# Optimization experiments

Hardware: AMD Instinct MI355X
Metric: run time of the kernel (lower is better)

Reference implementation:

```python
import jax, jax.numpy as jnp
import numpy as np
from jax import lax

B, N, F_IN, T = 4, 30000, 2, 12
HID, HORIZON, E = 32, 12, 240000


def setup_inputs() -> dict:
    key = jax.random.key(0)
    ks = jax.random.split(key, 20)

    def lin_init(k, fan_in, shape):
        b = 1.0 / np.sqrt(fan_in)
        return jax.random.uniform(k, shape, jnp.float32, -b, b)

    def glorot(k, shape):
        b = np.sqrt(6.0 / (shape[0] + shape[1]))
        return jax.random.uniform(k, shape, jnp.float32, -b, b)

    return {
        "x": jax.random.normal(ks[0], (B, N, F_IN, T), jnp.float32),
        "edge_index": jax.random.randint(ks[1], (2, E), 0, N, jnp.int32),
        # A3TGCN2 attention over periods (init: uniform[0,1))
        "attention": jax.random.uniform(ks[2], (T,), jnp.float32),
        # TGCN2 gates: GCNConv weight (F_IN,HID) + bias, Linear (2*HID,HID) + bias
        "conv_z_w": glorot(ks[3], (F_IN, HID)), "conv_z_b": jnp.zeros((HID,), jnp.float32),
        "lin_z_w": lin_init(ks[4], 2 * HID, (2 * HID, HID)), "lin_z_b": lin_init(ks[5], 2 * HID, (HID,)),
        "conv_r_w": glorot(ks[6], (F_IN, HID)), "conv_r_b": jnp.zeros((HID,), jnp.float32),
        "lin_r_w": lin_init(ks[7], 2 * HID, (2 * HID, HID)), "lin_r_b": lin_init(ks[8], 2 * HID, (HID,)),
        "conv_h_w": glorot(ks[9], (F_IN, HID)), "conv_h_b": jnp.zeros((HID,), jnp.float32),
        "lin_h_w": lin_init(ks[10], 2 * HID, (2 * HID, HID)), "lin_h_b": lin_init(ks[11], 2 * HID, (HID,)),
        # trailing head Linear(HID, HORIZON)
        "head_w": lin_init(ks[12], HID, (HID, HORIZON)), "head_b": lin_init(ks[13], HID, (HORIZON,)),
    }


def _forward(x, attention, conv_z_w, conv_z_b, lin_z_w, lin_z_b,
             conv_r_w, conv_r_b, lin_r_w, lin_r_b,
             conv_h_w, conv_h_b, lin_h_w, lin_h_b,
             head_w, head_b, edge_index):
    b, n = x.shape[0], x.shape[1]
    # GCN normalization with added self loops: D^-1/2 (A+I) D^-1/2
    loop = jnp.arange(n, dtype=edge_index.dtype)
    src = jnp.concatenate([edge_index[0], loop])  # (E+N,) message sources
    dst = jnp.concatenate([edge_index[1], loop])  # (E+N,) message targets
    deg = jnp.zeros((n,), x.dtype).at[dst].add(1.0)  # deg >= 1 due to self loops
    dinv = lax.rsqrt(deg)
    norm = dinv[src] * dinv[dst]  # (E+N,)

    def gcn(xt, W, bias):
        # xt: (B,N,F) -> (B,N,HID); gather from src, scatter-add to dst
        xw = jnp.einsum('bnf,fh->bnh', xt, W)
        msg = xw[:, src, :] * norm[None, :, None]  # (B,E+N,HID)
        agg = jnp.zeros((b, n, W.shape[1]), xt.dtype).at[:, dst, :].add(msg)
        return agg + bias

    probs = jax.nn.softmax(attention)  # (T,)
    H0 = jnp.zeros((b, n, HID), x.dtype)  # A3TGCN2 passes H=None every period

    def step(acc, inps):
        xt, p = inps  # xt: (B,N,F)
        Z = jax.nn.sigmoid(jnp.concatenate([gcn(xt, conv_z_w, conv_z_b), H0], -1) @ lin_z_w + lin_z_b)
        R = jax.nn.sigmoid(jnp.concatenate([gcn(xt, conv_r_w, conv_r_b), H0], -1) @ lin_r_w + lin_r_b)
        Ht = jnp.tanh(jnp.concatenate([gcn(xt, conv_h_w, conv_h_b), H0 * R], -1) @ lin_h_w + lin_h_b)
        Hn = Z * H0 + (1.0 - Z) * Ht
        return acc + p * Hn, None

    acc, _ = lax.scan(step, H0, (jnp.moveaxis(x, 3, 0), probs))
    return jax.nn.relu(acc) @ head_w + head_b  # (B,N,HORIZON)


def reference(x, edge_index, attention, conv_z_w, conv_z_b, lin_z_w, lin_z_b,
              conv_r_w, conv_r_b, lin_r_w, lin_r_b,
              conv_h_w, conv_h_b, lin_h_w, lin_h_b, head_w, head_b):
    return _forward(x, attention, conv_z_w, conv_z_b, lin_z_w, lin_z_b,
                    conv_r_w, conv_r_b, lin_r_w, lin_r_b,
                    conv_h_w, conv_h_b, lin_h_w, lin_h_b,
                    head_w, head_b, edge_index)
```

## Files before the change

kernel.cpp:

```cpp
#include <hip/hip_runtime.h>

#define BB   4
#define NN   30000
#define TT   12
#define EE   240000
#define FT   24
#define NM   96
#define CAP  32
#define OVCAP 2048
#define FB   ((EE + 255) / 256)
#define LOG2E 1.44269504088896340736f

#define WS_CNT 0
#define WS_OVC 30000
#define WS_EFF 30016
#define WS_OVF 30272
#define WS_BKT 34368

__device__ __forceinline__ float readlane_f(float v, int l) {
    return __int_as_float(__builtin_amdgcn_readlane(__float_as_int(v), l));
}

__global__ void __launch_bounds__(256)
k_pre(const int* __restrict__ src, const int* __restrict__ dst,
      const float* __restrict__ czw, const float* __restrict__ czb,
      const float* __restrict__ lzw, const float* __restrict__ lzb,
      const float* __restrict__ chw, const float* __restrict__ chb,
      const float* __restrict__ lhw, const float* __restrict__ lhb,
      const float* __restrict__ att,
      int* __restrict__ cnt, int* __restrict__ ovc,
      int* __restrict__ ovf, int* __restrict__ bucket, float* __restrict__ eff) {
    int bid = blockIdx.x, lt = threadIdx.x;
    if (bid < FB) {
        int e = bid * 256 + lt;
        if (e < EE) {
            int d = dst[e], s = src[e];
            int slot = atomicAdd(&cnt[d], 1);
            if (slot < CAP) {
                bucket[d * CAP + slot] = s;
            } else {
                int o = atomicAdd(ovc, 1);
                if (o < OVCAP) { ovf[2 * o] = d; ovf[2 * o + 1] = s; }
            }
        }
        return;
    }
    int j = lt;
    if (j < 32) {
        float wz0 = 0.f, wz1 = 0.f, bz = 0.f, wh0 = 0.f, wh1 = 0.f, bh = 0.f;
        for (int k = 0; k < 32; ++k) {
            float lz = lzw[k * 32 + j], lh = lhw[k * 32 + j];
            wz0 = fmaf(czw[k],      lz, wz0);
            wz1 = fmaf(czw[32 + k], lz, wz1);
            bz  = fmaf(czb[k],      lz, bz);
            wh0 = fmaf(chw[k],      lh, wh0);
            wh1 = fmaf(chw[32 + k], lh, wh1);
            bh  = fmaf(chb[k],      lh, bh);
        }
        eff[j]        = -LOG2E * wz0;
        eff[32 + j]   = -LOG2E * wz1;
        eff[64 + j]   = -LOG2E * (bz + lzb[j]);
        eff[96 + j]   = 2.0f * LOG2E * wh0;
        eff[128 + j]  = 2.0f * LOG2E * wh1;
        eff[160 + j]  = 2.0f * LOG2E * (bh + lhb[j]);
    } else if (j == 32) {
        float m = -1e30f;
        for (int t = 0; t < TT; ++t) m = fmaxf(m, att[t]);
        float p[TT], s = 0.f;
        for (int t = 0; t < TT; ++t) { p[t] = __expf(att[t] - m); s += p[t]; }
        float inv = 1.0f / s;
        for (int t = 0; t < TT; ++t) eff[192 + t] = p[t] * inv;
    }
}

__global__ void __launch_bounds__(128)
k_fused(const float* __restrict__ x, const int* __restrict__ cnt,
        const int* __restrict__ ovc, const int* __restrict__ ovf,
        const int* __restrict__ bucket, const float* __restrict__ eff,
        const float* __restrict__ hw, const float* __restrict__ hb,
        float* __restrict__ out) {
    __shared__ float se[204];
    __shared__ float shwT[432];
    __shared__ float shb[12];
    __shared__ float sx[2 * NM];
    __shared__ float lacc[2 * 4 * 36];
    const int lt = threadIdx.x, lane = lt & 63, w = lt >> 6;
    const int n = blockIdx.x * 2 + w;

    for (int i = lt; i < 204; i += 128) se[i] = eff[i];
    if (lt < 12) shb[lt] = hb[lt];
    for (int i = lt; i < 384; i += 128) {
        int jj = i / 12, kk = i - 12 * jj;
        shwT[kk * 36 + jj] = hw[i];
    }
    __syncthreads();

    const bool act = (lane < 48);
    const int b = lane / 12, f2 = lane - 12 * b;
    const float2* xb = (const float2*)x;
    const int lane_off = b * (NN * 12) + f2;

    const int deg = __builtin_amdgcn_readfirstlane(cnt[n]);
    const int m = (deg < CAP) ? deg : CAP;
    int sv = (lane < m) ? bucket[n * CAP + lane] : n;
    float wv = (lane <= m) ? rsqrtf((float)(cnt[sv] + 1)) : 0.f;

    float2 acc = {0.f, 0.f};
    const int total = m + 1;
    int k = 0;
    for (; k + 8 <= total; k += 8) {
        int s0 = __builtin_amdgcn_readlane(sv, k);
        int s1 = __builtin_amdgcn_readlane(sv, k + 1);
        int s2 = __builtin_amdgcn_readlane(sv, k + 2);
        int s3 = __builtin_amdgcn_readlane(sv, k + 3);
        int s4 = __builtin_amdgcn_readlane(sv, k + 4);
        int s5 = __builtin_amdgcn_readlane(sv, k + 5);
        int s6 = __builtin_amdgcn_readlane(sv, k + 6);
        int s7 = __builtin_amdgcn_readlane(sv, k + 7);
        if (act) {
            float2 v0 = xb[lane_off + s0 * 12];
            float2 v1 = xb[lane_off + s1 * 12];
            float2 v2 = xb[lane_off + s2 * 12];
            float2 v3 = xb[lane_off + s3 * 12];
            float2 v4 = xb[lane_off + s4 * 12];
            float2 v5 = xb[lane_off + s5 * 12];
            float2 v6 = xb[lane_off + s6 * 12];
            float2 v7 = xb[lane_off + s7 * 12];
            float w0 = readlane_f(wv, k),     w1 = readlane_f(wv, k + 1);
            float w2 = readlane_f(wv, k + 2), w3 = readlane_f(wv, k + 3);
            float w4 = readlane_f(wv, k + 4), w5 = readlane_f(wv, k + 5);
            float w6 = readlane_f(wv, k + 6), w7 = readlane_f(wv, k + 7);
            acc.x = fmaf(w0, v0.x, acc.x); acc.y = fmaf(w0, v0.y, acc.y);
            acc.x = fmaf(w1, v1.x, acc.x); acc.y = fmaf(w1, v1.y, acc.y);
            acc.x = fmaf(w2, v2.x, acc.x); acc.y = fmaf(w2, v2.y, acc.y);
            acc.x = fmaf(w3, v3.x, acc.x); acc.y = fmaf(w3, v3.y, acc.y);
            acc.x = fmaf(w4, v4.x, acc.x); acc.y = fmaf(w4, v4.y, acc.y);
            acc.x = fmaf(w5, v5.x, acc.x); acc.y = fmaf(w5, v5.y, acc.y);
            acc.x = fmaf(w6, v6.x, acc.x); acc.y = fmaf(w6, v6.y, acc.y);
            acc.x = fmaf(w7, v7.x, acc.x); acc.y = fmaf(w7, v7.y, acc.y);
        }
    }
    for (; k < total; k += 4) {
        int s0 = __builtin_amdgcn_readlane(sv, k);
        int s1 = __builtin_amdgcn_readlane(sv, k + 1);
        int s2 = __builtin_amdgcn_readlane(sv, k + 2);
        int s3 = __builtin_amdgcn_readlane(sv, k + 3);
        if (act) {
            float2 v0 = xb[lane_off + s0 * 12];
            float2 v1 = xb[lane_off + s1 * 12];
            float2 v2 = xb[lane_off + s2 * 12];
            float2 v3 = xb[lane_off + s3 * 12];
            float w0 = readlane_f(wv, k),     w1 = readlane_f(wv, k + 1);
            float w2 = readlane_f(wv, k + 2), w3 = readlane_f(wv, k + 3);
            acc.x = fmaf(w0, v0.x, acc.x); acc.y = fmaf(w0, v0.y, acc.y);
            acc.x = fmaf(w1, v1.x, acc.x); acc.y = fmaf(w1, v1.y, acc.y);
            acc.x = fmaf(w2, v2.x, acc.x); acc.y = fmaf(w2, v2.y, acc.y);
            acc.x = fmaf(w3, v3.x, acc.x); acc.y = fmaf(w3, v3.y, acc.y);
        }
    }

    int nov = __builtin_amdgcn_readfirstlane(*ovc);
    if (nov > 0) {
        if (nov > OVCAP) nov = OVCAP;
        for (int i = 0; i < nov; ++i) {
            int d = ovf[2 * i];
            if (d == n) {
                int s = ovf[2 * i + 1];
                float ws_ = rsqrtf((float)(cnt[s] + 1));
                if (act) {
                    float2 v = xb[lane_off + s * 12];
                    acc.x = fmaf(ws_, v.x, acc.x);
                    acc.y = fmaf(ws_, v.y, acc.y);
                }
            }
        }
    }

    const float dn = readlane_f(wv, m);
    if (act) {
        float2* sx2 = (float2*)(sx + w * NM + b * FT);
        sx2[f2] = make_float2(dn * acc.x, dn * acc.y);
    }
    __builtin_amdgcn_wave_barrier();

    const int j = lane & 31, b0_ = lane >> 5;
    const float az0 = se[j],      az1 = se[32 + j],  ab = se[64 + j];
    const float ch0 = se[96 + j], ch1 = se[128 + j], cb = se[160 + j];
#pragma unroll
    for (int bi = 0; bi < 2; ++bi) {
        const int bb = b0_ + 2 * bi;
        const float4* s4 = (const float4*)(sx + w * NM + bb * FT);
        float4 q[6];
#pragma unroll
        for (int i = 0; i < 6; ++i) q[i] = s4[i];
        const float* av = (const float*)q;
        float a = 0.f;
#pragma unroll
        for (int t = 0; t < TT; ++t) {
            float v0 = av[t], v1 = av[12 + t], pp = se[192 + t];
            float ae = fmaf(v1, az1, fmaf(v0, az0, ab));
            float ce = fmaf(v1, ch1, fmaf(v0, ch0, cb));
            ae = __builtin_amdgcn_fmed3f(ae, -126.f, 126.f);
            ce = __builtin_amdgcn_fmed3f(ce, -126.f, 126.f);
            float u  = __builtin_amdgcn_exp2f(ae);
            float e2 = __builtin_amdgcn_exp2f(ce);
            float t1_ = 1.0f + u;
            float den = fmaf(e2, t1_, t1_);
            float num = fmaf(u, e2, -u);
            float r   = __builtin_amdgcn_rcpf(den);
            a = fmaf(pp * num, r, a);
        }
        lacc[(w * 4 + bb) * 36 + j] = fmaxf(a, 0.f);
    }
    __builtin_amdgcn_wave_barrier();

    if (lane < 48) {
        int bb = lane / 12, kk = lane - 12 * bb;
        float r = shb[kk];
        const float4* la4 = (const float4*)(lacc + (w * 4 + bb) * 36);
        const float4* wt4 = (const float4*)(shwT + kk * 36);
#pragma unroll
        for (int i = 0; i < 8; ++i) {
            float4 a4 = la4[i], w4 = wt4[i];
            r = fmaf(a4.x, w4.x, r); r = fmaf(a4.y, w4.y, r);
            r = fmaf(a4.z, w4.z, r); r = fmaf(a4.w, w4.w, r);
        }
        out[((long long)bb * NN + n) * 12 + kk] = r;
    }
}

extern "C" void kernel_launch(void* const* d_in, const int* in_sizes, int n_in,
                              void* d_out, int out_size, void* d_ws, size_t ws_size,
                              hipStream_t stream) {
    const float* x   = (const float*)d_in[0];
    const int*   ei  = (const int*)d_in[1];
    const float* att = (const float*)d_in[2];
    const float* czw = (const float*)d_in[3];
    const float* czb = (const float*)d_in[4];
    const float* lzw = (const float*)d_in[5];
    const float* lzb = (const float*)d_in[6];
    const float* chw = (const float*)d_in[11];
    const float* chb = (const float*)d_in[12];
    const float* lhw = (const float*)d_in[13];
    const float* lhb = (const float*)d_in[14];
    const float* hw  = (const float*)d_in[15];
    const float* hb  = (const float*)d_in[16];
    float* out = (float*)d_out;

    float* ws = (float*)d_ws;
    int*   cnt = (int*)(ws + WS_CNT);
    int*   ovc = (int*)(ws + WS_OVC);
    float* eff = ws + WS_EFF;
    int*   ovf = (int*)(ws + WS_OVF);
    int*   bkt = (int*)(ws + WS_BKT);

    const int* src = ei;
    const int* dst = ei + EE;

    hipMemsetAsync(cnt, 0, WS_EFF * 4, stream);
    k_pre<<<FB + 1, 256, 0, stream>>>(src, dst, czw, czb, lzw, lzb,
                                      chw, chb, lhw, lhb, att,
                                      cnt, ovc, ovf, bkt, eff);
    k_fused<<<NN / 2, 128, 0, stream>>>(x, cnt, ovc, ovf, bkt, eff, hw, hb, out);
}
```

Baseline: 142.4 us.

## Prescale node features by inverse sqrt degree in a separate pass before aggregation

Adds a kernel that writes a copy of x scaled by each source node's rsqrt(degree) into workspace, with a zero padding row per batch. The fused kernel then sums gathered rows without per-edge weights, removing the dependent gather of cnt[src] and the per-neighbor rsqrt and readlane work. The cost is an extra kernel launch plus a full read and write of the x-sized tensor, and the separate pass splits what was one fused stage.

Result: slower. 146.8 us (+3.1%).

```diff
diff --git a/kernel.cpp b/kernel.cpp
--- a/kernel.cpp
+++ b/kernel.cpp
@@ -9,6 +9,7 @@
 #define CAP  32
 #define OVCAP 2048
 #define FB   ((EE + 255) / 256)
+#define MB   (BB * NN * FT / 256)
 #define LOG2E 1.44269504088896340736f
 
 #define WS_CNT 0
@@ -16,6 +17,7 @@
 #define WS_EFF 30016
 #define WS_OVF 30272
 #define WS_BKT 34368
+#define WS_Y   994368
 
 __device__ __forceinline__ float readlane_f(float v, int l) {
     return __int_as_float(__builtin_amdgcn_readlane(__float_as_int(v), l));
@@ -73,8 +75,27 @@
     }
 }
 
+__global__ void __launch_bounds__(256)
+k_mid(const float* __restrict__ x, const int* __restrict__ cnt,
+      float* __restrict__ y) {
+    int bid = blockIdx.x, lt = threadIdx.x;
+    if (bid < MB) {
+        int idx = bid * 256 + lt;
+        int ft = idx % FT;
+        int rest = idx / FT;
+        int n = rest % NN, b = rest / NN;
+        float di = rsqrtf((float)(cnt[n] + 1));
+        y[(b * (NN + 1) + n) * FT + ft] = x[idx] * di;
+        return;
+    }
+    if (lt < BB * FT) {
+        int b = lt / FT, ft = lt - FT * b;
+        y[(b * (NN + 1) + NN) * FT + ft] = 0.f;
+    }
+}
+
 __global__ void __launch_bounds__(128)
-k_fused(const float* __restrict__ x, const int* __restrict__ cnt,
+k_fused(const float* __restrict__ y, const int* __restrict__ cnt,
         const int* __restrict__ ovc, const int* __restrict__ ovf,
         const int* __restrict__ bucket, const float* __restrict__ eff,
         const float* __restrict__ hw, const float* __restrict__ hb,
@@ -97,13 +118,13 @@
 
     const bool act = (lane < 48);
     const int b = lane / 12, f2 = lane - 12 * b;
-    const float2* xb = (const float2*)x;
-    const int lane_off = b * (NN * 12) + f2;
+    const float2* yb = (const float2*)y;
+    const int lane_off = b * ((NN + 1) * 12) + f2;
 
     const int deg = __builtin_amdgcn_readfirstlane(cnt[n]);
     const int m = (deg < CAP) ? deg : CAP;
-    int sv = (lane < m) ? bucket[n * CAP + lane] : n;
-    float wv = (lane <= m) ? rsqrtf((float)(cnt[sv] + 1)) : 0.f;
+    const float dn = rsqrtf((float)(deg + 1));
+    int sv = (lane < m) ? bucket[n * CAP + lane] : ((lane == m) ? n : NN);
 
     float2 acc = {0.f, 0.f};
     const int total = m + 1;
@@ -118,26 +139,18 @@
         int s6 = __builtin_amdgcn_readlane(sv, k + 6);
         int s7 = __builtin_amdgcn_readlane(sv, k + 7);
         if (act) {
-            float2 v0 = xb[lane_off + s0 * 12];
-            float2 v1 = xb[lane_off + s1 * 12];
-            float2 v2 = xb[lane_off + s2 * 12];
-            float2 v3 = xb[lane_off + s3 * 12];
-            float2 v4 = xb[lane_off + s4 * 12];
-            float2 v5 = xb[lane_off + s5 * 12];
-            float2 v6 = xb[lane_off + s6 * 12];
-            float2 v7 = xb[lane_off + s7 * 12];
-            float w0 = readlane_f(wv, k),     w1 = readlane_f(wv, k + 1);
-            float w2 = readlane_f(wv, k + 2), w3 = readlane_f(wv, k + 3);
-            float w4 = readlane_f(wv, k + 4), w5 = readlane_f(wv, k + 5);
-            float w6 = readlane_f(wv, k + 6), w7 = readlane_f(wv, k + 7);
-            acc.x = fmaf(w0, v0.x, acc.x); acc.y = fmaf(w0, v0.y, acc.y);
-            acc.x = fmaf(w1, v1.x, acc.x); acc.y = fmaf(w1, v1.y, acc.y);
-            acc.x = fmaf(w2, v2.x, acc.x); acc.y = fmaf(w2, v2.y, acc.y);
-            acc.x = fmaf(w3, v3.x, acc.x); acc.y = fmaf(w3, v3.y, acc.y);
-            acc.x = fmaf(w4, v4.x, acc.x); acc.y = fmaf(w4, v4.y, acc.y);
-            acc.x = fmaf(w5, v5.x, acc.x); acc.y = fmaf(w5, v5.y, acc.y);
-            acc.x = fmaf(w6, v6.x, acc.x); acc.y = fmaf(w6, v6.y, acc.y);
-            acc.x = fmaf(w7, v7.x, acc.x); acc.y = fmaf(w7, v7.y, acc.y);
+            float2 v0 = yb[lane_off + s0 * 12];
+            float2 v1 = yb[lane_off + s1 * 12];
+            float2 v2 = yb[lane_off + s2 * 12];
+            float2 v3 = yb[lane_off + s3 * 12];
+            float2 v4 = yb[lane_off + s4 * 12];
+            float2 v5 = yb[lane_off + s5 * 12];
+            float2 v6 = yb[lane_off + s6 * 12];
+            float2 v7 = yb[lane_off + s7 * 12];
+            acc.x += v0.x + v1.x; acc.y += v0.y + v1.y;
+            acc.x += v2.x + v3.x; acc.y += v2.y + v3.y;
+            acc.x += v4.x + v5.x; acc.y += v4.y + v5.y;
+            acc.x += v6.x + v7.x; acc.y += v6.y + v7.y;
         }
     }
     for (; k < total; k += 4) {
@@ -146,16 +159,12 @@
         int s2 = __builtin_amdgcn_readlane(sv, k + 2);
         int s3 = __builtin_amdgcn_readlane(sv, k + 3);
         if (act) {
-            float2 v0 = xb[lane_off + s0 * 12];
-            float2 v1 = xb[lane_off + s1 * 12];
-            float2 v2 = xb[lane_off + s2 * 12];
-            float2 v3 = xb[lane_off + s3 * 12];
-            float w0 = readlane_f(wv, k),     w1 = readlane_f(wv, k + 1);
-            float w2 = readlane_f(wv, k + 2), w3 = readlane_f(wv, k + 3);
-            acc.x = fmaf(w0, v0.x, acc.x); acc.y = fmaf(w0, v0.y, acc.y);
-            acc.x = fmaf(w1, v1.x, acc.x); acc.y = fmaf(w1, v1.y, acc.y);
-            acc.x = fmaf(w2, v2.x, acc.x); acc.y = fmaf(w2, v2.y, acc.y);
-            acc.x = fmaf(w3, v3.x, acc.x); acc.y = fmaf(w3, v3.y, acc.y);
+            float2 v0 = yb[lane_off + s0 * 12];
+            float2 v1 = yb[lane_off + s1 * 12];
+            float2 v2 = yb[lane_off + s2 * 12];
+            float2 v3 = yb[lane_off + s3 * 12];
+            acc.x += v0.x + v1.x; acc.y += v0.y + v1.y;
+            acc.x += v2.x + v3.x; acc.y += v2.y + v3.y;
         }
     }
 
@@ -166,17 +175,14 @@
             int d = ovf[2 * i];
             if (d == n) {
                 int s = ovf[2 * i + 1];
-                float ws_ = rsqrtf((float)(cnt[s] + 1));
                 if (act) {
-                    float2 v = xb[lane_off + s * 12];
-                    acc.x = fmaf(ws_, v.x, acc.x);
-                    acc.y = fmaf(ws_, v.y, acc.y);
+                    float2 v = yb[lane_off + s * 12];
+                    acc.x += v.x; acc.y += v.y;
                 }
             }
         }
     }
 
-    const float dn = readlane_f(wv, m);
     if (act) {
         float2* sx2 = (float2*)(sx + w * NM + b * FT);
         sx2[f2] = make_float2(dn * acc.x, dn * acc.y);
@@ -253,6 +259,7 @@
     float* eff = ws + WS_EFF;
     int*   ovf = (int*)(ws + WS_OVF);
     int*   bkt = (int*)(ws + WS_BKT);
+    float* y   = ws + WS_Y;
 
     const int* src = ei;
     const int* dst = ei + EE;
@@ -261,5 +268,6 @@
     k_pre<<<FB + 1, 256, 0, stream>>>(src, dst, czw, czb, lzw, lzb,
                                       chw, chb, lhw, lhb, att,
                                       cnt, ovc, ovf, bkt, eff);
-    k_fused<<<NN / 2, 128, 0, stream>>>(x, cnt, ovc, ovf, bkt, eff, hw, hb, out);
-}
+    k_mid<<<MB + 1, 256, 0, stream>>>(x, cnt, y);
+    k_fused<<<NN / 2, 128, 0, stream>>>(y, cnt, ovc, ovf, bkt, eff, hw, hb, out);
+}
```
